# Kernel optimization log

Hardware: AMD Instinct MI355X
Metric: run time of the kernel (lower is better)

The kernel has to match this reference:

```python
import jax, jax.numpy as jnp
import numpy as np

B, S, D_IN, D_OUT = 8, 2048, 1024, 64


def setup_inputs() -> dict:
    key = jax.random.key(0)
    ks = jax.random.split(key, 8)
    seq = jax.random.normal(ks[0], (B, S, D_IN), dtype=jnp.float32)
    mask = jax.random.bernoulli(ks[1], 0.15, (B, S))  # True = masked out
    lim = 1.0 / np.sqrt(D_IN)
    Wq = jax.random.uniform(ks[2], (D_IN, D_OUT), jnp.float32, -lim, lim)
    bq = jax.random.uniform(ks[3], (D_OUT,), jnp.float32, -lim, lim)
    Wk = jax.random.uniform(ks[4], (D_IN, D_OUT), jnp.float32, -lim, lim)
    bk = jax.random.uniform(ks[5], (D_OUT,), jnp.float32, -lim, lim)
    Wv = jax.random.uniform(ks[6], (D_IN, D_OUT), jnp.float32, -lim, lim)
    bv = jax.random.uniform(ks[7], (D_OUT,), jnp.float32, -lim, lim)
    return {"seq": seq, "mask": mask, "Wq": Wq, "bq": bq, "Wk": Wk, "bk": bk, "Wv": Wv, "bv": bv}


def reference(seq, mask, Wq, bq, Wk, bk, Wv, bv):
    q = jnp.einsum('bsd,df->bsf', seq, Wq) + bq  # [B,S,D_OUT]
    k = jnp.einsum('bsd,df->bsf', seq, Wk) + bk
    v = jnp.einsum('bsd,df->bsf', seq, Wv) + bv
    # NOTE: original code scales by sqrt(query.shape[1]) == sqrt(S), not sqrt(d)
    scale = jnp.asarray(q.shape[1], q.dtype) ** 0.5
    scores = jnp.einsum('bqf,bkf->bqk', q, k) / scale  # [B,S,S]
    scores = jnp.where(mask[:, None, :], jnp.asarray(-1e9, scores.dtype), scores)
    attn = jax.nn.softmax(scores, axis=-1)
    context = jnp.einsum('bqk,bkf->bqf', attn, v)  # [B,S,D_OUT]
    return context
```

## Files before the change

### kernel.cpp

```cpp
#include <hip/hip_runtime.h>
#include <hip/hip_bf16.h>
#include <stdint.h>

#define NB 8
#define SS 2048
#define DIN 1024
#define DOUT 64
#define MTOT (NB*SS)
#define SCALE 0.02209708691207961f

typedef short  short8 __attribute__((ext_vector_type(8)));
typedef float  f32x4  __attribute__((ext_vector_type(4)));
typedef unsigned short us4 __attribute__((ext_vector_type(4)));

#define WT_OFF 0
#define FM_OFF 393216
#define Q_OFF  524288
#define K_OFF  (Q_OFF + MTOT*DOUT*2)
#define VT_OFF (K_OFF + MTOT*DOUT*2)

__device__ __forceinline__ short f2bf(float f) {
  __bf16 h = (__bf16)f;
  return __builtin_bit_cast(short, h);
}

__global__ void k_mask(const void* __restrict__ mraw, float* __restrict__ fm) {
  __shared__ int bad[2];
  int t = threadIdx.x;
  if (t < 2) bad[t] = 0;
  __syncthreads();
  const uint32_t* w = (const uint32_t*)mraw;
  int b0 = 0, b1 = 0;
  for (int i = t; i < 4096; i += 256) {
    uint32_t v = w[i];
    b0 |= !(v == 0u || v == 1u);
    b1 |= !(v == 0u || v == 0x3F800000u);
  }
  if (b0) atomicOr(&bad[0], 1);
  if (b1) atomicOr(&bad[1], 1);
  __syncthreads();
  int u8mode = bad[0] && bad[1];
  const uint8_t* p8 = (const uint8_t*)mraw;
  for (int i = t; i < MTOT; i += 256) {
    int mv = u8mode ? (p8[i] != 0) : (w[i] != 0u);
    fm[i] = mv ? 0.0f : 1.0f;
  }
}

__global__ void k_prepw(const float* __restrict__ Wq, const float* __restrict__ Wk,
                        const float* __restrict__ Wv, __bf16* __restrict__ Wt) {
  __shared__ float tile[64][65];
  int bid = blockIdx.x;
  int m = bid >> 4;
  int k0 = (bid & 15) * 64;
  const float* W = (m == 0) ? Wq : (m == 1 ? Wk : Wv);
  float sc = (m == 0) ? SCALE : 1.0f;
  int t = threadIdx.x;
  #pragma unroll
  for (int i = 0; i < 16; i++) {
    int idx = i*256 + t;
    tile[idx >> 6][idx & 63] = W[(size_t)(k0 + (idx >> 6))*DOUT + (idx & 63)] * sc;
  }
  __syncthreads();
  #pragma unroll
  for (int i = 0; i < 16; i++) {
    int idx = i*256 + t;
    int n = idx >> 6, kk = idx & 63;
    Wt[(size_t)(m*DOUT + n)*DIN + k0 + kk] = (__bf16)tile[kk][n];
  }
}

__global__ __launch_bounds__(256) void k_qkv(
    const float* __restrict__ seq, const __bf16* __restrict__ Wt,
    const float* __restrict__ bq, const float* __restrict__ bk,
    const float* __restrict__ bv,
    __bf16* __restrict__ Qo, __bf16* __restrict__ Ko, __bf16* __restrict__ Vto) {
  __shared__ uint8_t bsm[192*128];
  int t = threadIdx.x;
  int wave = t >> 6, lane = t & 63, lg = lane >> 4, ll = lane & 15;
  int m0 = blockIdx.x * 64;
  int arow = m0 + wave*16 + ll;
  const float* abase = seq + (size_t)arow * DIN;

  f32x4 acur[2][2];
  #pragma unroll
  for (int kk = 0; kk < 2; kk++) {
    const float* ap = abase + kk*32 + lg*8;
    acur[kk][0] = *(const f32x4*)(ap);
    acur[kk][1] = *(const f32x4*)(ap + 4);
  }
  f32x4 acc[12];
  #pragma unroll
  for (int i = 0; i < 12; i++) acc[i] = f32x4{0.f,0.f,0.f,0.f};

  for (int c = 0; c < 16; c++) {
    int k0 = c * 64;
    __syncthreads();
    #pragma unroll
    for (int j = 0; j < 6; j++) {
      int flat = j*256 + t;
      int R = flat >> 3, u = flat & 7;
      short8 v = *(const short8*)((const uint8_t*)Wt + (size_t)R*2048 + (size_t)k0*2 + u*16);
      *(short8*)(bsm + R*128 + ((u ^ (R & 7)) * 16)) = v;
    }
    __syncthreads();
    short8 ab[2];
    #pragma unroll
    for (int kk = 0; kk < 2; kk++)
      #pragma unroll
      for (int j = 0; j < 8; j++)
        ab[kk][j] = f2bf(j < 4 ? acur[kk][0][j] : acur[kk][1][j-4]);
    if (c < 15) {
      #pragma unroll
      for (int kk = 0; kk < 2; kk++) {
        const float* ap = abase + (k0 + 64) + kk*32 + lg*8;
        acur[kk][0] = *(const f32x4*)(ap);
        acur[kk][1] = *(const f32x4*)(ap + 4);
      }
    }
    #pragma unroll
    for (int kk = 0; kk < 2; kk++) {
      #pragma unroll
      for (int mm = 0; mm < 12; mm++) {
        int R = mm*16 + ll;
        int u = kk*4 + lg;
        short8 bb = *(const short8*)(bsm + R*128 + ((u ^ (R & 7)) * 16));
        acc[mm] = __builtin_amdgcn_mfma_f32_16x16x32_bf16(ab[kk], bb, acc[mm], 0, 0, 0);
      }
    }
  }
  int orow = m0 + wave*16 + lg*4;
  int bb_ = orow >> 11;
  int sloc = orow & 2047;
  #pragma unroll
  for (int mm = 0; mm < 12; mm++) {
    int mat = mm >> 2;
    int col = (mm & 3)*16 + ll;
    float bias = (mat == 0) ? bq[col]*SCALE : (mat == 1 ? bk[col] : bv[col]);
    if (mat == 0) {
      #pragma unroll
      for (int r = 0; r < 4; r++)
        Qo[(size_t)(orow + r)*DOUT + col] = (__bf16)(acc[mm][r] + bias);
    } else if (mat == 1) {
      #pragma unroll
      for (int r = 0; r < 4; r++)
        Ko[(size_t)(orow + r)*DOUT + col] = (__bf16)(acc[mm][r] + bias);
    } else {
      us4 pk;
      #pragma unroll
      for (int r = 0; r < 4; r++) pk[r] = (unsigned short)f2bf(acc[mm][r] + bias);
      *(us4*)((uint8_t*)Vto + ((size_t)(bb_*DOUT + col)*SS + sloc)*2) = pk;
    }
  }
}

__global__ __launch_bounds__(256) void k_attn(
    const __bf16* __restrict__ Q, const __bf16* __restrict__ Kd,
    const __bf16* __restrict__ Vt, const float* __restrict__ fm,
    float* __restrict__ out) {
  __shared__ uint8_t smem[57344];
  float* fml = (float*)(smem + 49152);
  int t = threadIdx.x, wave = t >> 6, lane = t & 63, lg = lane >> 4, ll = lane & 15;
  int b = blockIdx.x >> 5, qt = blockIdx.x & 31;
  int q0 = qt*64 + wave*16;

  for (int i = t; i < SS; i += 256) fml[i] = fm[b*SS + i];

  const uint8_t* qbase = (const uint8_t*)Q + ((size_t)(b*SS + q0 + ll))*128;
  short8 aq[2];
  aq[0] = *(const short8*)(qbase + lg*16);
  aq[1] = *(const short8*)(qbase + 64 + lg*16);

  f32x4 oacc[4];
  #pragma unroll
  for (int i = 0; i < 4; i++) oacc[i] = f32x4{0.f,0.f,0.f,0.f};
  float den[4] = {0.f, 0.f, 0.f, 0.f};

  const uint8_t* kgbase = (const uint8_t*)Kd + (size_t)b*SS*128;
  const uint8_t* vgbase = (const uint8_t*)Vt + (size_t)b*DOUT*SS*2;
  uint8_t* pbase = smem + 32768 + wave*4096;

  for (int kb = 0; kb < 16; kb++) {
    __syncthreads();
    #pragma unroll
    for (int j = 0; j < 4; j++) {
      int flat = j*256 + t;
      int key = flat >> 3, u = flat & 7;
      short8 v = *(const short8*)(kgbase + (size_t)(kb*128 + key)*128 + u*16);
      *(short8*)(smem + key*128 + ((u ^ (key & 7)) * 16)) = v;
    }
    #pragma unroll
    for (int j = 0; j < 4; j++) {
      int flat = j*256 + t;
      int d = flat >> 4, u = flat & 15;
      short8 v = *(const short8*)(vgbase + ((size_t)d*SS + kb*128)*2 + u*16);
      *(short8*)(smem + 16384 + d*256 + ((u ^ (d & 15)) * 16)) = v;
    }
    __syncthreads();
    f32x4 sacc[8];
    #pragma unroll
    for (int i = 0; i < 8; i++) sacc[i] = f32x4{0.f,0.f,0.f,0.f};
    #pragma unroll
    for (int kk = 0; kk < 2; kk++) {
      #pragma unroll
      for (int nf = 0; nf < 8; nf++) {
        int key = nf*16 + ll;
        int u = kk*4 + lg;
        short8 kf = *(const short8*)(smem + key*128 + ((u ^ (key & 7)) * 16));
        sacc[nf] = __builtin_amdgcn_mfma_f32_16x16x32_bf16(aq[kk], kf, sacc[nf], 0, 0, 0);
      }
    }
    #pragma unroll
    for (int nf = 0; nf < 8; nf++) {
      float msk = fml[kb*128 + nf*16 + ll];
      #pragma unroll
      for (int r = 0; r < 4; r++) {
        float p = msk * __expf(sacc[nf][r]);
        __bf16 pb = (__bf16)p;
        den[r] += (float)pb;
        int qrow = lg*4 + r;
        int col = nf*16 + ll;
        *(__bf16*)(pbase + qrow*256 + (((col >> 3) ^ qrow) * 16) + (col & 7)*2) = pb;
      }
    }
    #pragma unroll
    for (int ks = 0; ks < 4; ks++) {
      int u = ks*4 + lg;
      short8 pf = *(const short8*)(pbase + ll*256 + ((u ^ ll) * 16));
      #pragma unroll
      for (int df = 0; df < 4; df++) {
        int d = df*16 + ll;
        short8 vf = *(const short8*)(smem + 16384 + d*256 + ((u ^ (d & 15)) * 16));
        oacc[df] = __builtin_amdgcn_mfma_f32_16x16x32_bf16(pf, vf, oacc[df], 0, 0, 0);
      }
    }
  }
  #pragma unroll
  for (int r = 0; r < 4; r++) {
    float d = den[r];
    d += __shfl_xor(d, 1, 64);
    d += __shfl_xor(d, 2, 64);
    d += __shfl_xor(d, 4, 64);
    d += __shfl_xor(d, 8, 64);
    den[r] = d;
  }
  #pragma unroll
  for (int df = 0; df < 4; df++) {
    int col = df*16 + ll;
    #pragma unroll
    for (int r = 0; r < 4; r++) {
      int gq = b*SS + q0 + lg*4 + r;
      out[(size_t)gq*DOUT + col] = oacc[df][r] / den[r];
    }
  }
}

extern "C" void kernel_launch(void* const* d_in, const int* in_sizes, int n_in,
                              void* d_out, int out_size, void* d_ws, size_t ws_size,
                              hipStream_t stream) {
  const float* seq = (const float*)d_in[0];
  const void*  msk = d_in[1];
  const float* Wq  = (const float*)d_in[2];
  const float* bq  = (const float*)d_in[3];
  const float* Wk  = (const float*)d_in[4];
  const float* bk  = (const float*)d_in[5];
  const float* Wv  = (const float*)d_in[6];
  const float* bv  = (const float*)d_in[7];
  uint8_t* ws = (uint8_t*)d_ws;
  __bf16* Wt  = (__bf16*)(ws + WT_OFF);
  float*  fm  = (float*)(ws + FM_OFF);
  __bf16* Qb  = (__bf16*)(ws + Q_OFF);
  __bf16* Kb  = (__bf16*)(ws + K_OFF);
  __bf16* Vtb = (__bf16*)(ws + VT_OFF);
  float* out  = (float*)d_out;

  k_mask<<<dim3(1), dim3(256), 0, stream>>>(msk, fm);
  k_prepw<<<dim3(48), dim3(256), 0, stream>>>(Wq, Wk, Wv, Wt);
  k_qkv<<<dim3(256), dim3(256), 0, stream>>>(seq, Wt, bq, bk, bv, Qb, Kb, Vtb);
  k_attn<<<dim3(256), dim3(256), 0, stream>>>(Qb, Kb, Vtb, fm, out);
}
```

Measured before the change: 178.5 us.

## Double-buffer QKV and attention tiles with direct global-to-LDS async loads

Both the QKV projection and the attention kernel now stage their tiles with global_load_lds into two alternating LDS buffers. The next tile is prefetched while MFMAs run on the current one, which removes one barrier per iteration. The XOR swizzle moves from the LDS write to the global source address. The QKV kernel now stages fp32 seq rows in LDS instead of holding them in registers, which enlarges LDS use. Separately, the mask and weight-prep kernels are merged into one 112-block launch, and the mask conversion is spread across 64 blocks instead of one.

```diff
diff --git a/kernel.cpp b/kernel.cpp
--- a/kernel.cpp
+++ b/kernel.cpp
@@ -24,49 +24,53 @@
   return __builtin_bit_cast(short, h);
 }
 
-__global__ void k_mask(const void* __restrict__ mraw, float* __restrict__ fm) {
-  __shared__ int bad[2];
-  int t = threadIdx.x;
-  if (t < 2) bad[t] = 0;
-  __syncthreads();
-  const uint32_t* w = (const uint32_t*)mraw;
-  int b0 = 0, b1 = 0;
-  for (int i = t; i < 4096; i += 256) {
-    uint32_t v = w[i];
-    b0 |= !(v == 0u || v == 1u);
-    b1 |= !(v == 0u || v == 0x3F800000u);
-  }
-  if (b0) atomicOr(&bad[0], 1);
-  if (b1) atomicOr(&bad[1], 1);
-  __syncthreads();
-  int u8mode = bad[0] && bad[1];
-  const uint8_t* p8 = (const uint8_t*)mraw;
-  for (int i = t; i < MTOT; i += 256) {
+__device__ __forceinline__ void gl_lds16(const void* g, void* l) {
+  __builtin_amdgcn_global_load_lds(
+      (const __attribute__((address_space(1))) uint32_t*)g,
+      (__attribute__((address_space(3))) uint32_t*)l, 16, 0, 0);
+}
+
+__global__ void k_prep(const float* __restrict__ Wq, const float* __restrict__ Wk,
+                       const float* __restrict__ Wv, const void* __restrict__ mraw,
+                       __bf16* __restrict__ Wt, float* __restrict__ fm) {
+  int bid = blockIdx.x, t = threadIdx.x;
+  if (bid < 48) {
+    __shared__ float tile[64][65];
+    int m = bid >> 4;
+    int k0 = (bid & 15) * 64;
+    const float* W = (m == 0) ? Wq : (m == 1 ? Wk : Wv);
+    float sc = (m == 0) ? SCALE : 1.0f;
+    #pragma unroll
+    for (int i = 0; i < 16; i++) {
+      int idx = i*256 + t;
+      tile[idx >> 6][idx & 63] = W[(size_t)(k0 + (idx >> 6))*DOUT + (idx & 63)] * sc;
+    }
+    __syncthreads();
+    #pragma unroll
+    for (int i = 0; i < 16; i++) {
+      int idx = i*256 + t;
+      int n = idx >> 6, kk = idx & 63;
+      Wt[(size_t)(m*DOUT + n)*DIN + k0 + kk] = (__bf16)tile[kk][n];
+    }
+  } else {
+    __shared__ int bad[2];
+    if (t < 2) bad[t] = 0;
+    __syncthreads();
+    const uint32_t* w = (const uint32_t*)mraw;
+    int b0 = 0, b1 = 0;
+    for (int i = t; i < 4096; i += 256) {
+      uint32_t v = w[i];
+      b0 |= !(v == 0u || v == 1u);
+      b1 |= !(v == 0u || v == 0x3F800000u);
+    }
+    if (b0) atomicOr(&bad[0], 1);
+    if (b1) atomicOr(&bad[1], 1);
+    __syncthreads();
+    int u8mode = bad[0] && bad[1];
+    const uint8_t* p8 = (const uint8_t*)mraw;
+    int i = (bid - 48)*256 + t;
     int mv = u8mode ? (p8[i] != 0) : (w[i] != 0u);
     fm[i] = mv ? 0.0f : 1.0f;
-  }
-}
-
-__global__ void k_prepw(const float* __restrict__ Wq, const float* __restrict__ Wk,
-                        const float* __restrict__ Wv, __bf16* __restrict__ Wt) {
-  __shared__ float tile[64][65];
-  int bid = blockIdx.x;
-  int m = bid >> 4;
-  int k0 = (bid & 15) * 64;
-  const float* W = (m == 0) ? Wq : (m == 1 ? Wk : Wv);
-  float sc = (m == 0) ? SCALE : 1.0f;
-  int t = threadIdx.x;
-  #pragma unroll
-  for (int i = 0; i < 16; i++) {
-    int idx = i*256 + t;
-    tile[idx >> 6][idx & 63] = W[(size_t)(k0 + (idx >> 6))*DOUT + (idx & 63)] * sc;
-  }
-  __syncthreads();
-  #pragma unroll
-  for (int i = 0; i < 16; i++) {
-    int idx = i*256 + t;
-    int n = idx >> 6, kk = idx & 63;
-    Wt[(size_t)(m*DOUT + n)*DIN + k0 + kk] = (__bf16)tile[kk][n];
   }
 }
 
@@ -75,62 +79,67 @@
     const float* __restrict__ bq, const float* __restrict__ bk,
     const float* __restrict__ bv,
     __bf16* __restrict__ Qo, __bf16* __restrict__ Ko, __bf16* __restrict__ Vto) {
-  __shared__ uint8_t bsm[192*128];
-  int t = threadIdx.x;
-  int wave = t >> 6, lane = t & 63, lg = lane >> 4, ll = lane & 15;
+  __shared__ uint8_t smem[81920];
+  int t = threadIdx.x, w = t >> 6, lane = t & 63, lg = lane >> 4, ll = lane & 15;
   int m0 = blockIdx.x * 64;
-  int arow = m0 + wave*16 + ll;
-  const float* abase = seq + (size_t)arow * DIN;
-
-  f32x4 acur[2][2];
-  #pragma unroll
-  for (int kk = 0; kk < 2; kk++) {
-    const float* ap = abase + kk*32 + lg*8;
-    acur[kk][0] = *(const f32x4*)(ap);
-    acur[kk][1] = *(const f32x4*)(ap + 4);
-  }
+  const uint8_t* seqB = (const uint8_t*)seq;
+  const uint8_t* WtB  = (const uint8_t*)Wt;
+
   f32x4 acc[12];
   #pragma unroll
   for (int i = 0; i < 12; i++) acc[i] = f32x4{0.f,0.f,0.f,0.f};
 
+  auto STAGE = [&](int c) {
+    uint8_t* bufA = smem + (c & 1)*40960;
+    uint8_t* bufB = bufA + 16384;
+    #pragma unroll
+    for (int j = 0; j < 4; j++) {
+      int g = j*256 + w*64 + lane;
+      int r = g >> 4, u1 = g & 15;
+      int u = u1 ^ (((r & 7) << 1) | ((r >> 3) & 1));
+      gl_lds16(seqB + (size_t)(m0 + r)*4096 + c*256 + u*16,
+               bufA + (j*256 + w*64)*16);
+    }
+    #pragma unroll
+    for (int j = 0; j < 6; j++) {
+      int g = j*256 + w*64 + lane;
+      int R = g >> 3, u1 = g & 7;
+      int u = u1 ^ (R & 7);
+      gl_lds16(WtB + (size_t)R*2048 + c*128 + u*16,
+               bufB + (j*256 + w*64)*16);
+    }
+  };
+
+  STAGE(0);
+  __syncthreads();
   for (int c = 0; c < 16; c++) {
-    int k0 = c * 64;
-    __syncthreads();
-    #pragma unroll
-    for (int j = 0; j < 6; j++) {
-      int flat = j*256 + t;
-      int R = flat >> 3, u = flat & 7;
-      short8 v = *(const short8*)((const uint8_t*)Wt + (size_t)R*2048 + (size_t)k0*2 + u*16);
-      *(short8*)(bsm + R*128 + ((u ^ (R & 7)) * 16)) = v;
-    }
-    __syncthreads();
+    if (c < 15) STAGE(c + 1);
+    uint8_t* bufA = smem + (c & 1)*40960;
+    uint8_t* bufB = bufA + 16384;
+    int r = w*16 + ll;
+    int sa = ((r & 7) << 1) | ((r >> 3) & 1);
     short8 ab[2];
     #pragma unroll
-    for (int kk = 0; kk < 2; kk++)
-      #pragma unroll
-      for (int j = 0; j < 8; j++)
-        ab[kk][j] = f2bf(j < 4 ? acur[kk][0][j] : acur[kk][1][j-4]);
-    if (c < 15) {
-      #pragma unroll
-      for (int kk = 0; kk < 2; kk++) {
-        const float* ap = abase + (k0 + 64) + kk*32 + lg*8;
-        acur[kk][0] = *(const f32x4*)(ap);
-        acur[kk][1] = *(const f32x4*)(ap + 4);
-      }
+    for (int kk = 0; kk < 2; kk++) {
+      f32x4 a0 = *(const f32x4*)(bufA + r*256 + (((kk*8 + lg*2    ) ^ sa)*16));
+      f32x4 a1 = *(const f32x4*)(bufA + r*256 + (((kk*8 + lg*2 + 1) ^ sa)*16));
+      #pragma unroll
+      for (int j = 0; j < 4; j++) { ab[kk][j] = f2bf(a0[j]); ab[kk][4+j] = f2bf(a1[j]); }
     }
     #pragma unroll
     for (int kk = 0; kk < 2; kk++) {
       #pragma unroll
       for (int mm = 0; mm < 12; mm++) {
         int R = mm*16 + ll;
-        int u = kk*4 + lg;
-        short8 bb = *(const short8*)(bsm + R*128 + ((u ^ (R & 7)) * 16));
+        short8 bb = *(const short8*)(bufB + R*128 + (((kk*4 + lg) ^ (R & 7))*16));
         acc[mm] = __builtin_amdgcn_mfma_f32_16x16x32_bf16(ab[kk], bb, acc[mm], 0, 0, 0);
       }
     }
-  }
-  int orow = m0 + wave*16 + lg*4;
-  int bb_ = orow >> 11;
+    __syncthreads();
+  }
+
+  int orow = m0 + w*16 + lg*4;
+  int bb_  = orow >> 11;
   int sloc = orow & 2047;
   #pragma unroll
   for (int mm = 0; mm < 12; mm++) {
@@ -139,16 +148,16 @@
     float bias = (mat == 0) ? bq[col]*SCALE : (mat == 1 ? bk[col] : bv[col]);
     if (mat == 0) {
       #pragma unroll
-      for (int r = 0; r < 4; r++)
-        Qo[(size_t)(orow + r)*DOUT + col] = (__bf16)(acc[mm][r] + bias);
+      for (int rr = 0; rr < 4; rr++)
+        Qo[(size_t)(orow + rr)*DOUT + col] = (__bf16)(acc[mm][rr] + bias);
     } else if (mat == 1) {
       #pragma unroll
-      for (int r = 0; r < 4; r++)
-        Ko[(size_t)(orow + r)*DOUT + col] = (__bf16)(acc[mm][r] + bias);
+      for (int rr = 0; rr < 4; rr++)
+        Ko[(size_t)(orow + rr)*DOUT + col] = (__bf16)(acc[mm][rr] + bias);
     } else {
       us4 pk;
       #pragma unroll
-      for (int r = 0; r < 4; r++) pk[r] = (unsigned short)f2bf(acc[mm][r] + bias);
+      for (int rr = 0; rr < 4; rr++) pk[rr] = (unsigned short)f2bf(acc[mm][rr] + bias);
       *(us4*)((uint8_t*)Vto + ((size_t)(bb_*DOUT + col)*SS + sloc)*2) = pk;
     }
   }
@@ -158,11 +167,11 @@
     const __bf16* __restrict__ Q, const __bf16* __restrict__ Kd,
     const __bf16* __restrict__ Vt, const float* __restrict__ fm,
     float* __restrict__ out) {
-  __shared__ uint8_t smem[57344];
-  float* fml = (float*)(smem + 49152);
-  int t = threadIdx.x, wave = t >> 6, lane = t & 63, lg = lane >> 4, ll = lane & 15;
+  __shared__ uint8_t smem[90112];
+  float* fml = (float*)(smem + 81920);
+  int t = threadIdx.x, w = t >> 6, lane = t & 63, lg = lane >> 4, ll = lane & 15;
   int b = blockIdx.x >> 5, qt = blockIdx.x & 31;
-  int q0 = qt*64 + wave*16;
+  int q0 = qt*64 + w*16;
 
   for (int i = t; i < SS; i += 256) fml[i] = fm[b*SS + i];
 
@@ -176,27 +185,35 @@
   for (int i = 0; i < 4; i++) oacc[i] = f32x4{0.f,0.f,0.f,0.f};
   float den[4] = {0.f, 0.f, 0.f, 0.f};
 
-  const uint8_t* kgbase = (const uint8_t*)Kd + (size_t)b*SS*128;
-  const uint8_t* vgbase = (const uint8_t*)Vt + (size_t)b*DOUT*SS*2;
-  uint8_t* pbase = smem + 32768 + wave*4096;
-
+  const uint8_t* kgb = (const uint8_t*)Kd + (size_t)b*SS*128;
+  const uint8_t* vgb = (const uint8_t*)Vt + (size_t)b*DOUT*SS*2;
+  uint8_t* pbase = smem + 65536 + w*4096;
+
+  auto STAGE = [&](int kb, int bi) {
+    uint8_t* bk_ = smem + bi*32768;
+    uint8_t* bv_ = bk_ + 16384;
+    #pragma unroll
+    for (int j = 0; j < 4; j++) {
+      int g = j*256 + w*64 + lane;
+      int key = g >> 3, u1 = g & 7;
+      int u = u1 ^ (key & 7);
+      gl_lds16(kgb + (size_t)(kb*128 + key)*128 + u*16, bk_ + (j*256 + w*64)*16);
+    }
+    #pragma unroll
+    for (int j = 0; j < 4; j++) {
+      int g = j*256 + w*64 + lane;
+      int d = g >> 4, u1 = g & 15;
+      int u = u1 ^ (d & 15);
+      gl_lds16(vgb + (size_t)d*4096 + kb*256 + u*16, bv_ + (j*256 + w*64)*16);
+    }
+  };
+
+  STAGE(0, 0);
+  __syncthreads();
   for (int kb = 0; kb < 16; kb++) {
-    __syncthreads();
-    #pragma unroll
-    for (int j = 0; j < 4; j++) {
-      int flat = j*256 + t;
-      int key = flat >> 3, u = flat & 7;
-      short8 v = *(const short8*)(kgbase + (size_t)(kb*128 + key)*128 + u*16);
-      *(short8*)(smem + key*128 + ((u ^ (key & 7)) * 16)) = v;
-    }
-    #pragma unroll
-    for (int j = 0; j < 4; j++) {
-      int flat = j*256 + t;
-      int d = flat >> 4, u = flat & 15;
-      short8 v = *(const short8*)(vgbase + ((size_t)d*SS + kb*128)*2 + u*16);
-      *(short8*)(smem + 16384 + d*256 + ((u ^ (d & 15)) * 16)) = v;
-    }
-    __syncthreads();
+    if (kb < 15) STAGE(kb + 1, (kb + 1) & 1);
+    uint8_t* bk_ = smem + (kb & 1)*32768;
+    uint8_t* bv_ = bk_ + 16384;
     f32x4 sacc[8];
     #pragma unroll
     for (int i = 0; i < 8; i++) sacc[i] = f32x4{0.f,0.f,0.f,0.f};
@@ -205,8 +222,7 @@
       #pragma unroll
       for (int nf = 0; nf < 8; nf++) {
         int key = nf*16 + ll;
-        int u = kk*4 + lg;
-        short8 kf = *(const short8*)(smem + key*128 + ((u ^ (key & 7)) * 16));
+        short8 kf = *(const short8*)(bk_ + key*128 + (((kk*4 + lg) ^ (key & 7))*16));
         sacc[nf] = __builtin_amdgcn_mfma_f32_16x16x32_bf16(aq[kk], kf, sacc[nf], 0, 0, 0);
       }
     }
@@ -220,20 +236,21 @@
         den[r] += (float)pb;
         int qrow = lg*4 + r;
         int col = nf*16 + ll;
-        *(__bf16*)(pbase + qrow*256 + (((col >> 3) ^ qrow) * 16) + (col & 7)*2) = pb;
+        *(__bf16*)(pbase + qrow*256 + (((col >> 3) ^ qrow)*16) + (col & 7)*2) = pb;
       }
     }
     #pragma unroll
     for (int ks = 0; ks < 4; ks++) {
       int u = ks*4 + lg;
-      short8 pf = *(const short8*)(pbase + ll*256 + ((u ^ ll) * 16));
+      short8 pf = *(const short8*)(pbase + ll*256 + ((u ^ ll)*16));
       #pragma unroll
       for (int df = 0; df < 4; df++) {
         int d = df*16 + ll;
-        short8 vf = *(const short8*)(smem + 16384 + d*256 + ((u ^ (d & 15)) * 16));
+        short8 vf = *(const short8*)(bv_ + d*256 + ((u ^ (d & 15))*16));
         oacc[df] = __builtin_amdgcn_mfma_f32_16x16x32_bf16(pf, vf, oacc[df], 0, 0, 0);
       }
     }
+    __syncthreads();
   }
   #pragma unroll
   for (int r = 0; r < 4; r++) {
@@ -274,8 +291,7 @@
   __bf16* Vtb = (__bf16*)(ws + VT_OFF);
   float* out  = (float*)d_out;
 
-  k_mask<<<dim3(1), dim3(256), 0, stream>>>(msk, fm);
-  k_prepw<<<dim3(48), dim3(256), 0, stream>>>(Wq, Wk, Wv, Wt);
+  k_prep<<<dim3(112), dim3(256), 0, stream>>>(Wq, Wk, Wv, msk, Wt, fm);
   k_qkv<<<dim3(256), dim3(256), 0, stream>>>(seq, Wt, bq, bk, bv, Qb, Kb, Vtb);
   k_attn<<<dim3(256), dim3(256), 0, stream>>>(Qb, Kb, Vtb, fm, out);
 }
```

Measured after the change: 147.6 us. 1.21x faster.
